# Kernel optimization log

Measured on AMD Instinct MI355X. Metric: run time of the kernel, lower is better.

## Reference

```python
import jax, jax.numpy as jnp
import numpy as np

B, L, HID = 2, 2048, 2048
H, D = 16, 128
BASE = 10000.0
EPS = 1e-6
SOFT_CAP = 30.0
NEG = jnp.finfo(jnp.float32).min


def setup_inputs() -> dict:
    key = jax.random.key(0)
    ks = jax.random.split(key, 8)
    s = 0.02
    return {
        "hidden_states": jax.random.normal(ks[0], (B, L, HID), jnp.float32),
        "Wq": jax.random.normal(ks[1], (HID, HID), jnp.float32) * s,
        "Wk": jax.random.normal(ks[2], (HID, HID), jnp.float32) * s,
        "Wv": jax.random.normal(ks[3], (HID, HID), jnp.float32) * s,
        "Wo": jax.random.normal(ks[4], (HID, HID), jnp.float32) * s,
        "q_norm_w": jnp.zeros((HID,), jnp.float32),
        "k_norm_w": jnp.zeros((HID,), jnp.float32),
        "k_bias": jax.random.normal(ks[5], (H, D), jnp.float32) * s,
        "v_bias": jax.random.normal(ks[6], (H, D), jnp.float32) * s,
        "positions": jnp.broadcast_to(jnp.arange(L, dtype=jnp.int32), (B, L)),
        "attention_mask": jnp.ones((B, L, L), dtype=bool),
    }


def _rms_norm(x, w):
    var = jnp.mean(jnp.square(x.astype(jnp.float32)), axis=-1, keepdims=True)
    y = x * jax.lax.rsqrt(var + EPS)
    return ((1.0 + w) * y).astype(x.dtype)


def _rope(x, cos, sin):
    # x: [B, L, H, D]; cos/sin: [B, L, 1, D//2]; neox style
    x1, x2 = jnp.split(x, 2, axis=-1)
    return jnp.concatenate([x1 * cos - x2 * sin, x2 * cos + x1 * sin], axis=-1)


def reference(hidden_states, Wq, Wk, Wv, Wo, q_norm_w, k_norm_w, k_bias, v_bias,
              positions, attention_mask):
    fan_in = HID ** -0.5
    q = (hidden_states @ Wq.T) * fan_in
    k = (hidden_states @ Wk.T) * fan_in
    v = (hidden_states @ Wv.T) * fan_in

    # qk-norm on flat hidden dim (GiddRMSNorm over hidden_size)
    q = _rms_norm(q, q_norm_w)
    k = _rms_norm(k, k_norm_w)

    q = q.reshape(B, L, H, D)
    k = k.reshape(B, L, H, D)
    v = v.reshape(B, L, H, D)

    # rotary embedding (neox, rotary_dim == head_dim)
    inv = 1.0 / (BASE ** (jnp.arange(0, D, 2, dtype=jnp.float32) / D))  # [D//2]
    ang = positions.astype(jnp.float32)[..., None] * inv  # [B, L, D//2]
    cos = jnp.cos(ang)[:, :, None, :]
    sin = jnp.sin(ang)[:, :, None, :]
    q = _rope(q, cos, sin)
    k = _rope(k, cos, sin)

    # learned attention biases on k/v per head
    k = k + k_bias[None, None, :, :]
    v = v + v_bias[None, None, :, :]

    q = q.transpose(0, 2, 1, 3)  # [B, H, L, D]
    k = k.transpose(0, 2, 1, 3)
    v = v.transpose(0, 2, 1, 3)

    scale = D ** -0.5
    scores = jnp.einsum('bhqd,bhkd->bhqk', q * scale, k)
    scores = SOFT_CAP * jnp.tanh(scores / SOFT_CAP)
    scores = jnp.where(attention_mask[:, None, :, :], scores, NEG)
    probs = jax.nn.softmax(scores.astype(jnp.float32), axis=-1).astype(scores.dtype)
    out = jnp.einsum('bhqk,bhkd->bhqd', probs, v)
    out = out.transpose(0, 2, 1, 3).reshape(B, L, HID)
    return (out @ Wo.T) * fan_in
```

## Files before the change

### kernel.cpp

```cpp
#include <hip/hip_runtime.h>
#include <math.h>

#define B_  2
#define L_  2048
#define HID_ 2048
#define H_  16
#define D_  128
#define FAN_IN 0.02209708691207961f
#define SM_SCALE 0.08838834764831845f
#define LOG2E 1.4426950408889634

typedef _Float16 f16;
typedef unsigned int u32;
typedef __attribute__((ext_vector_type(4))) _Float16 f16x4;
typedef __attribute__((ext_vector_type(8))) _Float16 f16x8;
typedef __attribute__((ext_vector_type(4))) float f32x4;

#define CAP_C0 0.12751738960681625f
#define CAP_C1 (-3.690028637e-7f)
#define CAP_C2 (1.28121e-12f)
#define FIXED_M2 8.0f

__device__ __forceinline__ float fexp2(float x) {
#if __has_builtin(__builtin_amdgcn_exp2f)
    return __builtin_amdgcn_exp2f(x);
#else
    return exp2f(x);
#endif
}
__device__ __forceinline__ float frcp(float x) {
#if __has_builtin(__builtin_amdgcn_rcpf)
    return __builtin_amdgcn_rcpf(x);
#else
    return 1.0f / x;
#endif
}
__device__ __forceinline__ void gload_lds16(const void* g, void* l) {
#if __has_builtin(__builtin_amdgcn_global_load_lds)
    __builtin_amdgcn_global_load_lds(
        (const __attribute__((address_space(1))) u32*)g,
        (__attribute__((address_space(3))) u32*)l, 16, 0, 0);
#else
    *(uint4*)l = *(const uint4*)g;
#endif
}

__global__ __launch_bounds__(256) void cvt5(
    const float* __restrict__ s0, const float* __restrict__ s1,
    const float* __restrict__ s2, const float* __restrict__ s3,
    const float* __restrict__ s4,
    f16* __restrict__ d0, f16* __restrict__ d1, f16* __restrict__ d2,
    f16* __restrict__ d3, f16* __restrict__ d4, int n0, int nw)
{
    const int seg = blockIdx.y;
    const float* s = seg==0?s0:seg==1?s1:seg==2?s2:seg==3?s3:s4;
    f16* d = seg==0?d0:seg==1?d1:seg==2?d2:seg==3?d3:d4;
    const int n = (seg==0) ? n0 : nw;
    const int i = (blockIdx.x*256 + threadIdx.x)*8;
    if (i >= n) return;
    float4 a = *(const float4*)&s[i];
    float4 b = *(const float4*)&s[i+4];
    f16x8 o;
    o[0]=(f16)a.x; o[1]=(f16)a.y; o[2]=(f16)a.z; o[3]=(f16)a.w;
    o[4]=(f16)b.x; o[5]=(f16)b.y; o[6]=(f16)b.z; o[7]=(f16)b.w;
    *(f16x8*)&d[i] = o;
}

__global__ __launch_bounds__(256) void gemm16_qkv(
    const f16* __restrict__ A,
    const f16* __restrict__ B0, const f16* __restrict__ B1,
    const f16* __restrict__ B2,
    f16* __restrict__ C0, f16* __restrict__ C1, f16* __restrict__ C2,
    int M, int N, int K, float scale)
{
    const f16* Bw = blockIdx.z==0 ? B0 : blockIdx.z==1 ? B1 : B2;
    f16* Cout     = blockIdx.z==0 ? C0 : blockIdx.z==1 ? C1 : C2;

    __shared__ f16 As[128*32];
    __shared__ f16 Bs[128*32];
    const int t = threadIdx.x;
    const int w = t >> 6, l = t & 63;
    const int lane15 = l & 15, quad = l >> 4;
    const int m0 = blockIdx.y*128, n0 = blockIdx.x*128;
    const int wm = (w & 1)*64, wn = (w >> 1)*64;

    const int srow = t >> 2;
    const int scol = (t & 3) * 8;
    const f16* Ag = A  + (size_t)(m0 + srow)*K + scol;
    const f16* Bg = Bw + (size_t)(n0 + srow)*K + scol;
    f16* Al = As + t*8;
    f16* Bl = Bs + t*8;

    f32x4 acc[4][4] = {};
    for (int k0 = 0; k0 < K; k0 += 32) {
        gload_lds16(Ag + k0,                 Al);
        gload_lds16(Ag + (size_t)64*K + k0,  Al + 2048);
        gload_lds16(Bg + k0,                 Bl);
        gload_lds16(Bg + (size_t)64*K + k0,  Bl + 2048);
        __syncthreads();
        f16x8 af[4], bf[4];
#pragma unroll
        for (int i = 0; i < 4; i++) {
            af[i] = *(const f16x8*)&As[(wm + i*16 + lane15)*32 + quad*8];
            bf[i] = *(const f16x8*)&Bs[(wn + i*16 + lane15)*32 + quad*8];
        }
#pragma unroll
        for (int i = 0; i < 4; i++)
#pragma unroll
            for (int j = 0; j < 4; j++)
                acc[i][j] = __builtin_amdgcn_mfma_f32_16x16x32_f16(af[i], bf[j], acc[i][j], 0, 0, 0);
        __syncthreads();
    }
#pragma unroll
    for (int i = 0; i < 4; i++)
#pragma unroll
        for (int j = 0; j < 4; j++) {
            const int col = n0 + wn + j*16 + lane15;
#pragma unroll
            for (int r = 0; r < 4; r++) {
                const int row = m0 + wm + i*16 + quad*4 + r;
                Cout[(size_t)row*N + col] = (f16)(acc[i][j][r] * scale);
            }
        }
}

__global__ __launch_bounds__(256) void gemm16_f32out(
    const f16* __restrict__ A, const f16* __restrict__ Bw,
    float* __restrict__ Cout, int M, int N, int K, float scale)
{
    __shared__ f16 As[128*32];
    __shared__ f16 Bs[128*32];
    const int t = threadIdx.x;
    const int w = t >> 6, l = t & 63;
    const int lane15 = l & 15, quad = l >> 4;
    const int m0 = blockIdx.y*128, n0 = blockIdx.x*128;
    const int wm = (w & 1)*64, wn = (w >> 1)*64;

    const int srow = t >> 2;
    const int scol = (t & 3) * 8;
    const f16* Ag = A  + (size_t)(m0 + srow)*K + scol;
    const f16* Bg = Bw + (size_t)(n0 + srow)*K + scol;
    f16* Al = As + t*8;
    f16* Bl = Bs + t*8;

    f32x4 acc[4][4] = {};
    for (int k0 = 0; k0 < K; k0 += 32) {
        gload_lds16(Ag + k0,                 Al);
        gload_lds16(Ag + (size_t)64*K + k0,  Al + 2048);
        gload_lds16(Bg + k0,                 Bl);
        gload_lds16(Bg + (size_t)64*K + k0,  Bl + 2048);
        __syncthreads();
        f16x8 af[4], bf[4];
#pragma unroll
        for (int i = 0; i < 4; i++) {
            af[i] = *(const f16x8*)&As[(wm + i*16 + lane15)*32 + quad*8];
            bf[i] = *(const f16x8*)&Bs[(wn + i*16 + lane15)*32 + quad*8];
        }
#pragma unroll
        for (int i = 0; i < 4; i++)
#pragma unroll
            for (int j = 0; j < 4; j++)
                acc[i][j] = __builtin_amdgcn_mfma_f32_16x16x32_f16(af[i], bf[j], acc[i][j], 0, 0, 0);
        __syncthreads();
    }
#pragma unroll
    for (int i = 0; i < 4; i++)
#pragma unroll
        for (int j = 0; j < 4; j++) {
            const int col = n0 + wn + j*16 + lane15;
#pragma unroll
            for (int r = 0; r < 4; r++) {
                const int row = m0 + wm + i*16 + quad*4 + r;
                Cout[(size_t)row*N + col] = acc[i][j][r] * scale;
            }
        }
}

__global__ void rope_table(const int* __restrict__ pos,
                           float* __restrict__ ct, float* __restrict__ st_)
{
    const int r = blockIdx.x, i = threadIdx.x;
    double inv = exp2(-(double)i * (13.287712379549449 / 64.0));
    double a = (double)pos[r] * inv;
    double sd, cd;
    sincos(a, &sd, &cd);
    ct[r*64+i] = (float)cd;
    st_[r*64+i] = (float)sd;
}

__global__ __launch_bounds__(256) void mask_pack(const int* __restrict__ m,
                                                 u32* __restrict__ bits)
{
    const int g = blockIdx.x*256 + threadIdx.x;
    const int* p = m + (size_t)g*32;
    u32 w = 0;
#pragma unroll
    for (int j = 0; j < 8; j++) {
        int4 v = *(const int4*)&p[j*4];
        w |= (v.x!=0 ? 1u:0u) << (j*4+0);
        w |= (v.y!=0 ? 1u:0u) << (j*4+1);
        w |= (v.z!=0 ? 1u:0u) << (j*4+2);
        w |= (v.w!=0 ? 1u:0u) << (j*4+3);
    }
    bits[g] = w;
}

__global__ __launch_bounds__(256) void norm_rope(
    f16* __restrict__ Q, f16* __restrict__ K,
    const float* __restrict__ qw, const float* __restrict__ kw,
    const float* __restrict__ kb,
    const float* __restrict__ ct, const float* __restrict__ st_)
{
    const int r = blockIdx.x;
    const int t = threadIdx.x;
    const size_t base = (size_t)r * HID_;

    const int p0 = t * 4;
    const int hh = p0 >> 6;
    const int i0 = p0 & 63;
    const int c1 = hh * 128 + i0;
    f16x4 q1h = *(f16x4*)&Q[base + c1];
    f16x4 q2h = *(f16x4*)&Q[base + c1 + 64];
    f16x4 k1h = *(f16x4*)&K[base + c1];
    f16x4 k2h = *(f16x4*)&K[base + c1 + 64];
    float q1[4], q2[4], k1[4], k2[4];
#pragma unroll
    for (int j = 0; j < 4; j++) {
        q1[j]=(float)q1h[j]; q2[j]=(float)q2h[j];
        k1[j]=(float)k1h[j]; k2[j]=(float)k2h[j];
    }

    float ssq = 0.f, ssk = 0.f;
#pragma unroll
    for (int j = 0; j < 4; j++) {
        ssq += q1[j]*q1[j] + q2[j]*q2[j];
        ssk += k1[j]*k1[j] + k2[j]*k2[j];
    }
#pragma unroll
    for (int off = 1; off < 64; off <<= 1) {
        ssq += __shfl_xor(ssq, off);
        ssk += __shfl_xor(ssk, off);
    }
    __shared__ float rq[4], rk[4];
    const int wave = t >> 6, lane = t & 63;
    if (lane == 0) { rq[wave] = ssq; rk[wave] = ssk; }
    __syncthreads();
    ssq = rq[0] + rq[1] + rq[2] + rq[3];
    ssk = rk[0] + rk[1] + rk[2] + rk[3];
    const float rsq = rsqrtf(ssq * (1.f / HID_) + 1e-6f);
    const float rsk = rsqrtf(ssk * (1.f / HID_) + 1e-6f);

    float4 cos4 = *(const float4*)&ct[r*64 + i0];
    float4 sin4 = *(const float4*)&st_[r*64 + i0];
    float cc[4] = {cos4.x, cos4.y, cos4.z, cos4.w};
    float ss[4] = {sin4.x, sin4.y, sin4.z, sin4.w};

    f16x4 oq1, oq2, ok1, ok2;
#pragma unroll
    for (int j = 0; j < 4; j++) {
        const float c = cc[j], s = ss[j];
        const float wq1 = 1.f + qw[c1 + j], wq2 = 1.f + qw[c1 + 64 + j];
        const float wk1 = 1.f + kw[c1 + j], wk2 = 1.f + kw[c1 + 64 + j];
        float qa = q1[j] * rsq * wq1, qb = q2[j] * rsq * wq2;
        oq1[j] = (f16)(qa * c - qb * s);
        oq2[j] = (f16)(qb * c + qa * s);
        float ka = k1[j] * rsk * wk1, kbv = k2[j] * rsk * wk2;
        ok1[j] = (f16)(ka * c - kbv * s + kb[c1 + j]);
        ok2[j] = (f16)(kbv * c + ka * s + kb[c1 + 64 + j]);
    }
    *(f16x4*)&Q[base + c1]      = oq1;
    *(f16x4*)&Q[base + c1 + 64] = oq2;
    *(f16x4*)&K[base + c1]      = ok1;
    *(f16x4*)&K[base + c1 + 64] = ok2;
}

__global__ __launch_bounds__(256) void vtrans(
    const f16* __restrict__ V, const float* __restrict__ vb,
    f16* __restrict__ Vt)
{
    __shared__ f16 tile[64][136];
    const int t = threadIdx.x;
    const int bh = blockIdx.y, lt = blockIdx.x;
    const int b = bh >> 4, h = bh & 15;
    const int l0 = lt * 64;
#pragma unroll
    for (int i = 0; i < 4; i++) {
        int f = t + i*256;
        int row = f >> 4, ch = f & 15;
        f16x8 v = *(const f16x8*)&V[((size_t)(b*L_ + l0 + row))*HID_ + h*128 + ch*8];
        f16x8 o;
#pragma unroll
        for (int j = 0; j < 8; j++)
            o[j] = (f16)((float)v[j] + vb[h*128 + ch*8 + j]);
        *(f16x8*)&tile[row][ch*8] = o;
    }
    __syncthreads();
#pragma unroll
    for (int i = 0; i < 4; i++) {
        int f = t + i*256;
        int d = f >> 3, ch = f & 7;
        f16x8 o;
#pragma unroll
        for (int j = 0; j < 8; j++) o[j] = tile[ch*8 + j][d];
        *(f16x8*)&Vt[((size_t)(bh*128 + d))*L_ + l0 + ch*8] = o;
    }
}

__global__ __launch_bounds__(256, 2) void flash16(
    const f16* __restrict__ Qh, const f16* __restrict__ Kh,
    const f16* __restrict__ Vtg, const u32* __restrict__ bits,
    f16* __restrict__ AOh)
{
    __shared__ f16 lds[40960];

    const int t = threadIdx.x;
    const int w = t >> 6, l = t & 63;
    const int lane15 = l & 15, quad = l >> 4;
    const int bh = blockIdx.y;
    const int b = bh >> 4, h = bh & 15;
    const int q0 = blockIdx.x * 128;

    const size_t qkbase = ((size_t)(b*L_))*HID_ + h*128;
    const size_t vbase  = ((size_t)(bh*128))*L_;

#pragma unroll
    for (int i = 0; i < 8; i++) {
        int f = t + i*256;
        int row = f >> 4, c4 = f & 15;
        int c = c4 ^ (row & 15);
        *(uint4*)&lds[row*128 + c4*8] =
            *(const uint4*)&Qh[qkbase + (size_t)(q0 + row)*HID_ + c*8];
    }
    __syncthreads();
    f16x8 qf[2][4];
#pragma unroll
    for (int qt = 0; qt < 2; qt++)
#pragma unroll
        for (int dc = 0; dc < 4; dc++)
            qf[qt][dc] = *(const f16x8*)&lds[(w*32 + qt*16 + lane15)*128
                                             + (((dc*4 + quad) ^ lane15) * 8)];
    __syncthreads();

    {
        f16* Kb = lds;            f16* Vb = lds + 16384;
#pragma unroll
        for (int it = 0; it < 4; it++) {
            int j = w*256 + it*64 + l;
            int krow = j >> 4, kc = (j & 15) ^ (krow & 15);
            gload_lds16(Kh + qkbase + (size_t)krow*HID_ + kc*8, Kb + j*8);
            int vrow = j >> 3, vc = (j & 7) ^ (vrow & 7);
            gload_lds16(Vtg + vbase + (size_t)vrow*L_ + vc*8, Vb + j*8);
        }
    }

    f32x4 oacc[2][8] = {};
    float lsum[2] = {0.f, 0.f};

    for (int kt = 0; kt < 32; kt++) {
        const int k0 = kt * 64;
        __syncthreads();

        if (kt + 1 < 32) {
            const int kn = k0 + 64;
            f16* Kb = lds + ((kt+1) & 1)*8192;
            f16* Vb = lds + 16384 + ((kt+1) & 1)*8192;
#pragma unroll
            for (int it = 0; it < 4; it++) {
                int j = w*256 + it*64 + l;
                int krow = j >> 4, kc = (j & 15) ^ (krow & 15);
                gload_lds16(Kh + qkbase + (size_t)(kn + krow)*HID_ + kc*8, Kb + j*8);
                int vrow = j >> 3, vc = (j & 7) ^ (vrow & 7);
                gload_lds16(Vtg + vbase + (size_t)vrow*L_ + kn + vc*8, Vb + j*8);
            }
        }
        const f16* Kb = lds + (kt & 1)*8192;
        const f16* Vb = lds + 16384 + (kt & 1)*8192;
        f16* Ps = lds + 32768;

        u32 mw[2][2];
#pragma unroll
        for (int qt = 0; qt < 2; qt++) {
            int qrow = q0 + w*32 + qt*16 + lane15;
            const u32* bp = bits + (((size_t)(b*L_ + qrow)) << 6) + (k0 >> 5);
            mw[qt][0] = bp[0];
            mw[qt][1] = bp[1];
        }

        f32x4 st[2][4];
#pragma unroll
        for (int kt2 = 0; kt2 < 4; kt2++) {
            f16x8 kf[4];
#pragma unroll
            for (int dc = 0; dc < 4; dc++)
                kf[dc] = *(const f16x8*)&Kb[(kt2*16 + lane15)*128
                                            + (((dc*4 + quad) ^ lane15) * 8)];
#pragma unroll
            for (int qt = 0; qt < 2; qt++) {
                f32x4 a = {0.f, 0.f, 0.f, 0.f};
#pragma unroll
                for (int dc = 0; dc < 4; dc++)
                    a = __builtin_amdgcn_mfma_f32_16x16x32_f16(kf[dc], qf[qt][dc], a, 0, 0, 0);
                st[qt][kt2] = a;
            }
        }

#pragma unroll
        for (int qt = 0; qt < 2; qt++) {
            const int prow = (w*32 + qt*16 + lane15) * 64;
            float ls = 0.f;
#pragma unroll
            for (int kt2 = 0; kt2 < 4; kt2++) {
                const u32 w_ = mw[qt][kt2 >> 1];
                f16x4 ph;
#pragma unroll
                for (int r = 0; r < 4; r++) {
                    float x = st[qt][kt2][r];
                    float y = x * x;
                    float p5 = fmaf(CAP_C2, y, CAP_C1);
                    float wv = fmaf(p5, y, CAP_C0);
                    float e = fmaf(x, wv, -FIXED_M2);
                    int kk = kt2*16 + quad*4 + r;
                    e = ((w_ >> (kk & 31)) & 1u) ? e : -150.f;
                    float pv = fexp2(e);
                    ls += pv;
                    ph[r] = (f16)pv;
                }
                const int c16s = (kt2*2 + (quad >> 1)) ^ (lane15 & 7);
                *(f16x4*)&Ps[prow + c16s*8 + (quad & 1)*4] = ph;
            }
            lsum[qt] += ls;
        }

        f16x8 pf[2][2];
#pragma unroll
        for (int qt = 0; qt < 2; qt++)
#pragma unroll
            for (int c = 0; c < 2; c++)
                pf[qt][c] = *(const f16x8*)&Ps[(w*32 + qt*16 + lane15)*64
                                               + (((c*4 + quad) ^ (lane15 & 7)) * 8)];
#pragma unroll
        for (int dt = 0; dt < 8; dt++) {
            f16x8 vf[2];
#pragma unroll
            for (int c = 0; c < 2; c++)
                vf[c] = *(const f16x8*)&Vb[(dt*16 + lane15)*64
                                           + (((c*4 + quad) ^ (lane15 & 7)) * 8)];
#pragma unroll
            for (int qt = 0; qt < 2; qt++)
#pragma unroll
                for (int c = 0; c < 2; c++)
                    oacc[qt][dt] = __builtin_amdgcn_mfma_f32_16x16x32_f16(pf[qt][c], vf[c], oacc[qt][dt], 0, 0, 0);
        }
    }

#pragma unroll
    for (int qt = 0; qt < 2; qt++) {
        lsum[qt] += __shfl_xor(lsum[qt], 16);
        lsum[qt] += __shfl_xor(lsum[qt], 32);
    }
    __syncthreads();
    f16* Ot = lds;
#pragma unroll
    for (int qt = 0; qt < 2; qt++) {
#pragma unroll
        for (int r = 0; r < 4; r++) {
            float inv = frcp(__shfl(lsum[qt], quad*4 + r));
            const int row = w*32 + qt*16 + quad*4 + r;
#pragma unroll
            for (int dt = 0; dt < 8; dt++)
                Ot[row*136 + dt*16 + lane15] = (f16)(oacc[qt][dt][r] * inv);
        }
    }
    __syncthreads();
#pragma unroll
    for (int i = 0; i < 8; i++) {
        int f = t + i*256;
        int row = f >> 4, ch = f & 15;
        *(uint4*)&AOh[qkbase + (size_t)(q0 + row)*HID_ + ch*8] =
            *(const uint4*)&Ot[row*136 + ch*8];
    }
}

extern "C" void kernel_launch(void* const* d_in, const int* in_sizes, int n_in,
                              void* d_out, int out_size, void* d_ws, size_t ws_size,
                              hipStream_t stream)
{
    const float* hs  = (const float*)d_in[0];
    const float* Wq  = (const float*)d_in[1];
    const float* Wk  = (const float*)d_in[2];
    const float* Wv  = (const float*)d_in[3];
    const float* Wo  = (const float*)d_in[4];
    const float* qw  = (const float*)d_in[5];
    const float* kw  = (const float*)d_in[6];
    const float* kb  = (const float*)d_in[7];
    const float* vb  = (const float*)d_in[8];
    const int*   pos = (const int*)d_in[9];
    const int*   mask = (const int*)d_in[10];
    float* out = (float*)d_out;

    char* W = (char*)d_ws;
    f16* hs16 = (f16*)(W);
    f16* w16o = (f16*)(W + 16777216);
    f16* w16q = (f16*)(W + 25165824);
    f16* w16k = (f16*)(W + 33554432);
    f16* w16v = (f16*)(W + 41943040);
    f16* Q16  = (f16*)(W + 50331648);
    f16* K16  = (f16*)(W + 67108864);
    f16* V16  = (f16*)(W + 83886080);
    f16* Vtg  = w16q;
    float* ct  = (float*)(W + 41943040);
    float* st_ = (float*)(W + 41943040 + 1048576);
    u32*  bits = (u32*) (W + 41943040 + 2097152);
    f16* AOh = hs16;

    const int M = B_ * L_;
    const int nHS = M * HID_;
    const int nW  = HID_ * HID_;

    cvt5<<<dim3(4096, 5), 256, 0, stream>>>(hs, Wq, Wk, Wv, Wo,
                                            hs16, w16q, w16k, w16v, w16o, nHS, nW);

    gemm16_qkv<<<dim3(HID_/128, M/128, 3), 256, 0, stream>>>(
        hs16, w16q, w16k, w16v, Q16, K16, V16, M, HID_, HID_, FAN_IN);

    rope_table<<<M, 64, 0, stream>>>(pos, ct, st_);
    mask_pack<<<1024, 256, 0, stream>>>(mask, bits);

    norm_rope<<<M, 256, 0, stream>>>(Q16, K16, qw, kw, kb, ct, st_);
    vtrans<<<dim3(32, 32), 256, 0, stream>>>(V16, vb, Vtg);

    flash16<<<dim3(16, 32), 256, 0, stream>>>(Q16, K16, Vtg, bits, AOh);

    gemm16_f32out<<<dim3(HID_/128, M/128), 256, 0, stream>>>(
        AOh, w16o, out, M, HID_, HID_, FAN_IN);
}
```

Before: 498.2 us.

## Fuse V bias and transpose into QKV GEMM epilogue; swizzle GEMM LDS

The QKV GEMM now writes the V projection directly in transposed per-head layout, adding the v bias in its epilogue, and the separate vtrans kernel is removed. This drops one kernel launch and a full read and write of V through global memory. Both GEMMs also gain an XOR swizzle on the LDS tile column chunks to reduce bank conflicts on the fragment reads. The transposed epilogue issues 8-byte stores strided by L, which coalesce less well than the old row-major stores.

```diff
diff --git a/kernel.cpp b/kernel.cpp
--- a/kernel.cpp
+++ b/kernel.cpp
@@ -70,11 +70,11 @@
     const f16* __restrict__ A,
     const f16* __restrict__ B0, const f16* __restrict__ B1,
     const f16* __restrict__ B2,
-    f16* __restrict__ C0, f16* __restrict__ C1, f16* __restrict__ C2,
+    f16* __restrict__ C0, f16* __restrict__ C1,
+    f16* __restrict__ Vt, const float* __restrict__ vb,
     int M, int N, int K, float scale)
 {
     const f16* Bw = blockIdx.z==0 ? B0 : blockIdx.z==1 ? B1 : B2;
-    f16* Cout     = blockIdx.z==0 ? C0 : blockIdx.z==1 ? C1 : C2;
 
     __shared__ f16 As[128*32];
     __shared__ f16 Bs[128*32];
@@ -85,7 +85,7 @@
     const int wm = (w & 1)*64, wn = (w >> 1)*64;
 
     const int srow = t >> 2;
-    const int scol = (t & 3) * 8;
+    const int scol = (((t & 3) ^ ((t >> 3) & 3))) * 8;
     const f16* Ag = A  + (size_t)(m0 + srow)*K + scol;
     const f16* Bg = Bw + (size_t)(n0 + srow)*K + scol;
     f16* Al = As + t*8;
@@ -101,8 +101,10 @@
         f16x8 af[4], bf[4];
 #pragma unroll
         for (int i = 0; i < 4; i++) {
-            af[i] = *(const f16x8*)&As[(wm + i*16 + lane15)*32 + quad*8];
-            bf[i] = *(const f16x8*)&Bs[(wn + i*16 + lane15)*32 + quad*8];
+            const int ra = wm + i*16 + lane15;
+            const int rb = wn + i*16 + lane15;
+            af[i] = *(const f16x8*)&As[ra*32 + ((quad ^ ((ra >> 1) & 3)) * 8)];
+            bf[i] = *(const f16x8*)&Bs[rb*32 + ((quad ^ ((rb >> 1) & 3)) * 8)];
         }
 #pragma unroll
         for (int i = 0; i < 4; i++)
@@ -111,17 +113,37 @@
                 acc[i][j] = __builtin_amdgcn_mfma_f32_16x16x32_f16(af[i], bf[j], acc[i][j], 0, 0, 0);
         __syncthreads();
     }
-#pragma unroll
-    for (int i = 0; i < 4; i++)
-#pragma unroll
-        for (int j = 0; j < 4; j++) {
-            const int col = n0 + wn + j*16 + lane15;
-#pragma unroll
-            for (int r = 0; r < 4; r++) {
-                const int row = m0 + wm + i*16 + quad*4 + r;
-                Cout[(size_t)row*N + col] = (f16)(acc[i][j][r] * scale);
+
+    if (blockIdx.z == 2) {
+#pragma unroll
+        for (int i = 0; i < 4; i++)
+#pragma unroll
+            for (int j = 0; j < 4; j++) {
+                const int col = n0 + wn + j*16 + lane15;
+                const int row0 = m0 + wm + i*16 + quad*4;
+                const int b = row0 >> 11, ll = row0 & 2047;
+                const int bh = (b << 4) + (col >> 7);
+                const float bias = vb[col];
+                f16x4 ph;
+#pragma unroll
+                for (int r = 0; r < 4; r++)
+                    ph[r] = (f16)(acc[i][j][r] * scale + bias);
+                *(f16x4*)&Vt[((size_t)(bh*128 + (col & 127)))*(size_t)L_ + ll] = ph;
             }
-        }
+    } else {
+        f16* Cout = blockIdx.z==0 ? C0 : C1;
+#pragma unroll
+        for (int i = 0; i < 4; i++)
+#pragma unroll
+            for (int j = 0; j < 4; j++) {
+                const int col = n0 + wn + j*16 + lane15;
+#pragma unroll
+                for (int r = 0; r < 4; r++) {
+                    const int row = m0 + wm + i*16 + quad*4 + r;
+                    Cout[(size_t)row*N + col] = (f16)(acc[i][j][r] * scale);
+                }
+            }
+    }
 }
 
 __global__ __launch_bounds__(256) void gemm16_f32out(
@@ -137,7 +159,7 @@
     const int wm = (w & 1)*64, wn = (w >> 1)*64;
 
     const int srow = t >> 2;
-    const int scol = (t & 3) * 8;
+    const int scol = (((t & 3) ^ ((t >> 3) & 3))) * 8;
     const f16* Ag = A  + (size_t)(m0 + srow)*K + scol;
     const f16* Bg = Bw + (size_t)(n0 + srow)*K + scol;
     f16* Al = As + t*8;
@@ -153,8 +175,10 @@
         f16x8 af[4], bf[4];
 #pragma unroll
         for (int i = 0; i < 4; i++) {
-            af[i] = *(const f16x8*)&As[(wm + i*16 + lane15)*32 + quad*8];
-            bf[i] = *(const f16x8*)&Bs[(wn + i*16 + lane15)*32 + quad*8];
+            const int ra = wm + i*16 + lane15;
+            const int rb = wn + i*16 + lane15;
+            af[i] = *(const f16x8*)&As[ra*32 + ((quad ^ ((ra >> 1) & 3)) * 8)];
+            bf[i] = *(const f16x8*)&Bs[rb*32 + ((quad ^ ((rb >> 1) & 3)) * 8)];
         }
 #pragma unroll
         for (int i = 0; i < 4; i++)
@@ -272,38 +296,6 @@
     *(f16x4*)&Q[base + c1 + 64] = oq2;
     *(f16x4*)&K[base + c1]      = ok1;
     *(f16x4*)&K[base + c1 + 64] = ok2;
-}
-
-__global__ __launch_bounds__(256) void vtrans(
-    const f16* __restrict__ V, const float* __restrict__ vb,
-    f16* __restrict__ Vt)
-{
-    __shared__ f16 tile[64][136];
-    const int t = threadIdx.x;
-    const int bh = blockIdx.y, lt = blockIdx.x;
-    const int b = bh >> 4, h = bh & 15;
-    const int l0 = lt * 64;
-#pragma unroll
-    for (int i = 0; i < 4; i++) {
-        int f = t + i*256;
-        int row = f >> 4, ch = f & 15;
-        f16x8 v = *(const f16x8*)&V[((size_t)(b*L_ + l0 + row))*HID_ + h*128 + ch*8];
-        f16x8 o;
-#pragma unroll
-        for (int j = 0; j < 8; j++)
-            o[j] = (f16)((float)v[j] + vb[h*128 + ch*8 + j]);
-        *(f16x8*)&tile[row][ch*8] = o;
-    }
-    __syncthreads();
-#pragma unroll
-    for (int i = 0; i < 4; i++) {
-        int f = t + i*256;
-        int d = f >> 3, ch = f & 7;
-        f16x8 o;
-#pragma unroll
-        for (int j = 0; j < 8; j++) o[j] = tile[ch*8 + j][d];
-        *(f16x8*)&Vt[((size_t)(bh*128 + d))*L_ + l0 + ch*8] = o;
-    }
 }
 
 __global__ __launch_bounds__(256, 2) void flash16(
@@ -506,8 +498,7 @@
     f16* w16v = (f16*)(W + 41943040);
     f16* Q16  = (f16*)(W + 50331648);
     f16* K16  = (f16*)(W + 67108864);
-    f16* V16  = (f16*)(W + 83886080);
-    f16* Vtg  = w16q;
+    f16* Vtg  = (f16*)(W + 83886080);
     float* ct  = (float*)(W + 41943040);
     float* st_ = (float*)(W + 41943040 + 1048576);
     u32*  bits = (u32*) (W + 41943040 + 2097152);
@@ -521,13 +512,12 @@
                                             hs16, w16q, w16k, w16v, w16o, nHS, nW);
 
     gemm16_qkv<<<dim3(HID_/128, M/128, 3), 256, 0, stream>>>(
-        hs16, w16q, w16k, w16v, Q16, K16, V16, M, HID_, HID_, FAN_IN);
+        hs16, w16q, w16k, w16v, Q16, K16, Vtg, vb, M, HID_, HID_, FAN_IN);
 
     rope_table<<<M, 64, 0, stream>>>(pos, ct, st_);
     mask_pack<<<1024, 256, 0, stream>>>(mask, bits);
 
     norm_rope<<<M, 256, 0, stream>>>(Q16, K16, qw, kw, kb, ct, st_);
-    vtrans<<<dim3(32, 32), 256, 0, stream>>>(V16, vb, Vtg);
 
     flash16<<<dim3(16, 32), 256, 0, stream>>>(Q16, K16, Vtg, bits, AOh);
 
```

After: 464.2 us. -6.8%, faster.
